# Performance work log

Measured on AMD Instinct MI355X. Metric: run time of the kernel, lower is better.

The kernel has to match this reference:

```python
import jax, jax.numpy as jnp
import numpy as np

B, T, E, H = 64, 577, 768, 64
GRID_H, GRID_W = 24, 24
NUM_PREFIX = 1
N = GRID_H * GRID_W  # 576 patches
EPS = 1e-5


def setup_inputs() -> dict:
    key = jax.random.key(0)
    ks = jax.random.split(key, 12)
    s = lambda k, shape, fan: jax.random.normal(k, shape, jnp.float32) / np.sqrt(fan)
    return {
        "x": jax.random.normal(ks[0], (B, T, E), jnp.float32),
        "w_q": s(ks[1], (E, H), E),
        "w_k": s(ks[2], (E, H), E),
        "w_v": s(ks[3], (E, H), E),
        "q_gamma": jnp.ones((H,), jnp.float32),
        "q_beta": jnp.zeros((H,), jnp.float32),
        "k_gamma": jnp.ones((H,), jnp.float32),
        "k_beta": jnp.zeros((H,), jnp.float32),
        "w_sigma": s(ks[4], (H, 2), H),
        "b_sigma": jnp.zeros((2,), jnp.float32),
        "w_alpha": s(ks[5], (H, 1), H),
        "b_alpha": jnp.zeros((1,), jnp.float32),
    }


def _layernorm(x, gamma, beta):
    mu = jnp.mean(x, axis=-1, keepdims=True)
    var = jnp.mean(jnp.square(x - mu), axis=-1, keepdims=True)
    return (x - mu) * jax.lax.rsqrt(var + EPS) * gamma + beta


def _grid_sq_dists():
    # coords[i] = (row, col) of patch i; squared coordinate differences [N, N]
    coords = jnp.stack(
        jnp.meshgrid(jnp.arange(GRID_H), jnp.arange(GRID_W), indexing="ij"), axis=-1
    ).reshape(N, 2).astype(jnp.float32)
    diff = coords[:, None, :] - coords[None, :, :]  # [N, N, 2]
    dy2 = jnp.square(diff[..., 0])  # row diff squared
    dx2 = jnp.square(diff[..., 1])  # col diff squared
    return dx2, dy2


def reference(x, w_q, w_k, w_v, q_gamma, q_beta, k_gamma, k_beta,
              w_sigma, b_sigma, w_alpha, b_alpha):
    q = _layernorm(x @ w_q, q_gamma, q_beta)  # [B, T, H]
    k = _layernorm(x @ w_k, k_gamma, k_beta)  # [B, T, H]
    v = x @ w_v                               # [B, T, H]

    sim = jnp.einsum("bqh,bkh->bqk", q, k)    # [B, T, T]

    q_nc = q[:, NUM_PREFIX:, :]               # [B, N, H]
    alpha = jax.nn.softplus(q_nc @ w_alpha + b_alpha)[..., 0]  # [B, N]
    sigma = jax.nn.sigmoid(q_nc @ w_sigma + b_sigma)           # [B, N, 2]
    sx = sigma[..., 0]  # [B, N]
    sy = sigma[..., 1]

    dx2, dy2 = _grid_sq_dists()  # [N, N] each
    # Gaussian decay bias: query-patch p controls sigma; [B, N, N]
    G = jnp.exp(
        -dx2[None] / (2.0 * jnp.square(sx)[:, :, None])
        - dy2[None] / (2.0 * jnp.square(sy)[:, :, None])
    )
    S = alpha[:, :, None] * G

    sim = sim.at[:, NUM_PREFIX:, NUM_PREFIX:].add(S)

    scale = jnp.sqrt(jnp.float32(H))
    attn = jax.nn.softmax(sim / scale, axis=-1)
    return attn @ v  # [B, T, H]
```

## Files before the change

kernel.cpp:

```cpp
#include <hip/hip_runtime.h>
#include <math.h>

#define B_ 64
#define T_ 577
#define E_ 768
#define H_ 64
#define N_ 576
#define GW_ 24

typedef float f32x4 __attribute__((ext_vector_type(4)));
typedef __bf16 bf16x8 __attribute__((ext_vector_type(8)));
typedef __bf16 bf16x4 __attribute__((ext_vector_type(4)));

__device__ inline void split_bf16(float f, __bf16& h, __bf16& l) {
  h = (__bf16)f;
  l = (__bf16)(f - (float)h);
}

__global__ __launch_bounds__(256) void prep_w_kernel(
    const float* __restrict__ wq, const float* __restrict__ wk, const float* __restrict__ wv,
    __bf16* __restrict__ wsw_hi, __bf16* __restrict__ wsw_lo)
{
  int t = blockIdx.x * 256 + threadIdx.x;
  if (t >= 24*192) return;
  int kc = t / 192, n = t - (t/192)*192;
  const float* src = (n < 64) ? wq : ((n < 128) ? wk : wv);
  int nn = n & 63;
  __bf16 hbuf[32], lbuf[32];
  #pragma unroll
  for (int kk = 0; kk < 32; ++kk) {
    float f = src[(size_t)(kc*32 + kk)*64 + nn];
    split_bf16(f, hbuf[kk], lbuf[kk]);
  }
  size_t base = (size_t)t * 32;
  #pragma unroll
  for (int i = 0; i < 4; ++i) {
    *(bf16x8*)(wsw_hi + base + i*8) = *(bf16x8*)&hbuf[i*8];
    *(bf16x8*)(wsw_lo + base + i*8) = *(bf16x8*)&lbuf[i*8];
  }
}

__global__ __launch_bounds__(256) void qkv_ln_kernel(
    const float* __restrict__ x,
    const __bf16* __restrict__ wsw_hi, const __bf16* __restrict__ wsw_lo,
    const float* __restrict__ qg, const float* __restrict__ qb,
    const float* __restrict__ kg, const float* __restrict__ kb,
    const float* __restrict__ wsig, const float* __restrict__ bsig,
    const float* __restrict__ walp, const float* __restrict__ balp,
    float* __restrict__ qo, float* __restrict__ ko, float* __restrict__ vo,
    float* __restrict__ alo, float* __restrict__ sxo, float* __restrict__ syo)
{
  __shared__ __align__(16) float smem[64*193 + 256];
  __bf16* A_hi = (__bf16*)smem;
  __bf16* A_lo = A_hi + 64*40;
  __bf16* B_hi = A_lo + 64*40;
  __bf16* B_lo = B_hi + 192*40;
  float (*Cs)[193] = (float (*)[193])smem;
  float* mu_q = smem + 64*193;
  float* rs_q = mu_q + 64;
  float* mu_k = rs_q + 64;
  float* rs_k = mu_k + 64;

  const int tid  = threadIdx.x;
  const int lane = tid & 63;
  const int w    = tid >> 6;
  const int rowbase = blockIdx.x << 6;

  f32x4 acc[4][3];
  #pragma unroll
  for (int mt = 0; mt < 4; ++mt)
    #pragma unroll
    for (int nt = 0; nt < 3; ++nt)
      acc[mt][nt] = (f32x4){0.f, 0.f, 0.f, 0.f};

  const int m     = lane & 15;
  const int kfrag = (lane >> 4) * 8;

  float4 xr0, xr1;
  bf16x8 whr[3], wlr[3];
  const int s0 = tid, s1 = tid + 256;
  const int arow0 = s0 >> 3, ak0 = (s0 & 7) * 4;
  const int arow1 = s1 >> 3, ak1 = (s1 & 7) * 4;

  auto load_chunk = [&](int kc) {
    xr0 = *(const float4*)(x + (size_t)(rowbase + arow0)*E_ + kc*32 + ak0);
    xr1 = *(const float4*)(x + (size_t)(rowbase + arow1)*E_ + kc*32 + ak1);
    #pragma unroll
    for (int i = 0; i < 3; ++i) {
      int e = tid + 256*i;
      whr[i] = *(const bf16x8*)(wsw_hi + (size_t)kc*6144 + e*8);
      wlr[i] = *(const bf16x8*)(wsw_lo + (size_t)kc*6144 + e*8);
    }
  };
  auto store_chunk = [&]() {
    __bf16 h0,l0,h1,l1,h2,l2,h3,l3;
    split_bf16(xr0.x,h0,l0); split_bf16(xr0.y,h1,l1);
    split_bf16(xr0.z,h2,l2); split_bf16(xr0.w,h3,l3);
    *(bf16x4*)&A_hi[arow0*40 + ak0] = (bf16x4){h0,h1,h2,h3};
    *(bf16x4*)&A_lo[arow0*40 + ak0] = (bf16x4){l0,l1,l2,l3};
    split_bf16(xr1.x,h0,l0); split_bf16(xr1.y,h1,l1);
    split_bf16(xr1.z,h2,l2); split_bf16(xr1.w,h3,l3);
    *(bf16x4*)&A_hi[arow1*40 + ak1] = (bf16x4){h0,h1,h2,h3};
    *(bf16x4*)&A_lo[arow1*40 + ak1] = (bf16x4){l0,l1,l2,l3};
    #pragma unroll
    for (int i = 0; i < 3; ++i) {
      int e = tid + 256*i;
      int n = e >> 2, g = e & 3;
      *(bf16x8*)&B_hi[n*40 + g*8] = whr[i];
      *(bf16x8*)&B_lo[n*40 + g*8] = wlr[i];
    }
  };

  load_chunk(0);
  #pragma unroll 1
  for (int kc = 0; kc < 24; ++kc) {
    __syncthreads();
    store_chunk();
    __syncthreads();
    if (kc < 23) load_chunk(kc + 1);

    bf16x8 bh[3], bl[3];
    #pragma unroll
    for (int nt = 0; nt < 3; ++nt) {
      int n = w*48 + nt*16 + m;
      bh[nt] = *(const bf16x8*)&B_hi[n*40 + kfrag];
      bl[nt] = *(const bf16x8*)&B_lo[n*40 + kfrag];
    }
    #pragma unroll
    for (int mt = 0; mt < 4; ++mt) {
      bf16x8 ah = *(const bf16x8*)&A_hi[(mt*16 + m)*40 + kfrag];
      bf16x8 al = *(const bf16x8*)&A_lo[(mt*16 + m)*40 + kfrag];
      #pragma unroll
      for (int nt = 0; nt < 3; ++nt) {
        acc[mt][nt] = __builtin_amdgcn_mfma_f32_16x16x32_bf16(ah, bh[nt], acc[mt][nt], 0, 0, 0);
        acc[mt][nt] = __builtin_amdgcn_mfma_f32_16x16x32_bf16(al, bh[nt], acc[mt][nt], 0, 0, 0);
        acc[mt][nt] = __builtin_amdgcn_mfma_f32_16x16x32_bf16(ah, bl[nt], acc[mt][nt], 0, 0, 0);
      }
    }
  }
  __syncthreads();

  #pragma unroll
  for (int mt = 0; mt < 4; ++mt)
    #pragma unroll
    for (int nt = 0; nt < 3; ++nt) {
      int row = mt*16 + (lane >> 4)*4;
      int col = w*48 + nt*16 + (lane & 15);
      Cs[row + 0][col] = acc[mt][nt].x;
      Cs[row + 1][col] = acc[mt][nt].y;
      Cs[row + 2][col] = acc[mt][nt].z;
      Cs[row + 3][col] = acc[mt][nt].w;
    }
  __syncthreads();

  if (tid < 64) {
    float s = 0.f;
    for (int h = 0; h < 64; ++h) s += Cs[tid][h];
    float mu = s * (1.f/64.f);
    float vs = 0.f;
    for (int h = 0; h < 64; ++h) { float d = Cs[tid][h] - mu; vs += d*d; }
    mu_q[tid] = mu;
    rs_q[tid] = rsqrtf(vs*(1.f/64.f) + 1e-5f);
  } else if (tid < 128) {
    int r = tid - 64;
    float s = 0.f;
    for (int h = 0; h < 64; ++h) s += Cs[r][64+h];
    float mu = s * (1.f/64.f);
    float vs = 0.f;
    for (int h = 0; h < 64; ++h) { float d = Cs[r][64+h] - mu; vs += d*d; }
    mu_k[r] = mu;
    rs_k[r] = rsqrtf(vs*(1.f/64.f) + 1e-5f);
  }
  __syncthreads();

  if (tid >= 192) {
    int r = tid - 192;
    int mrow = rowbase + r;
    int tindex = mrow % T_;
    if (tindex >= 1) {
      int bb = mrow / T_;
      int g = tindex - 1;
      float mu = mu_q[r], rs = rs_q[r];
      float za = 0.f, z0 = 0.f, z1 = 0.f;
      for (int h = 0; h < 64; ++h) {
        float qv = (Cs[r][h] - mu) * rs * qg[h] + qb[h];
        za += qv * walp[h];
        z0 += qv * wsig[2*h];
        z1 += qv * wsig[2*h+1];
      }
      za += balp[0]; z0 += bsig[0]; z1 += bsig[1];
      float al = fmaxf(za, 0.f) + log1pf(__expf(-fabsf(za)));
      float sx = 1.f/(1.f + __expf(-z0));
      float sy = 1.f/(1.f + __expf(-z1));
      alo[bb*N_ + g] = al;
      sxo[bb*N_ + g] = 0.5f/(sx*sx);
      syo[bb*N_ + g] = 0.5f/(sy*sy);
    }
  }
  for (int idx = tid; idx < 64*48; idx += 256) {
    int r = idx / 48, c4 = (idx - (idx/48)*48) * 4;
    size_t row = (size_t)rowbase + r;
    float4 val = make_float4(Cs[r][c4], Cs[r][c4+1], Cs[r][c4+2], Cs[r][c4+3]);
    if (c4 < 64) {
      float mu = mu_q[r], rs = rs_q[r];
      float4 o;
      o.x = (val.x - mu)*rs*qg[c4+0] + qb[c4+0];
      o.y = (val.y - mu)*rs*qg[c4+1] + qb[c4+1];
      o.z = (val.z - mu)*rs*qg[c4+2] + qb[c4+2];
      o.w = (val.w - mu)*rs*qg[c4+3] + qb[c4+3];
      *(float4*)(qo + row*64 + c4) = o;
    } else if (c4 < 128) {
      int h = c4 - 64;
      float mu = mu_k[r], rs = rs_k[r];
      float4 o;
      o.x = (val.x - mu)*rs*kg[h+0] + kb[h+0];
      o.y = (val.y - mu)*rs*kg[h+1] + kb[h+1];
      o.z = (val.z - mu)*rs*kg[h+2] + kb[h+2];
      o.w = (val.w - mu)*rs*kg[h+3] + kb[h+3];
      *(float4*)(ko + row*64 + h) = o;
    } else {
      *(float4*)(vo + row*64 + (c4-128)) = val;
    }
  }
}

__global__ __launch_bounds__(256) void attn_kernel(
    const float* __restrict__ q, const float* __restrict__ k, const float* __restrict__ v,
    const float* __restrict__ ala, const float* __restrict__ sxa, const float* __restrict__ sya,
    float* __restrict__ out)
{
  __shared__ __align__(16) __bf16 sm[8*4608];
  __shared__ float prm_al[64], prm_sx[64], prm_sy[64], prm_gr[64], prm_gc[64];
  __shared__ int   prm_has[64];

  __bf16* QH = sm;            __bf16* QL = sm + 4608;
  __bf16* KH = sm + 2*4608;   __bf16* KL = sm + 3*4608;
  __bf16* VH = sm + 4*4608;   __bf16* VL = sm + 5*4608;
  __bf16* PH = sm + 6*4608;   __bf16* PL = sm + 7*4608;

  const int tid  = threadIdx.x;
  const int lane = tid & 63;
  const int w    = tid >> 6;
  const int quad = lane >> 4;
  const int mrow = lane & 15;
  const int b    = blockIdx.y;
  const int qt   = blockIdx.x;

  const float* qbase = q + (size_t)b * T_ * H_;
  const float* kbase = k + (size_t)b * T_ * H_;
  const float* vbase = v + (size_t)b * T_ * H_;

  if (tid < 64) {
    int row = qt*64 + tid;
    float al=0.f, isx=0.f, isy=0.f, gr=0.f, gc=0.f; int has = 0;
    if (row >= 1 && row < T_) {
      int g = row - 1;
      al  = ala[b*N_ + g] * 0.125f;
      isx = sxa[b*N_ + g];
      isy = sya[b*N_ + g];
      gr  = (float)(g / GW_);
      gc  = (float)(g - (g/GW_)*GW_);
      has = 1;
    }
    prm_al[tid]=al; prm_sx[tid]=isx; prm_sy[tid]=isy;
    prm_gr[tid]=gr; prm_gc[tid]=gc; prm_has[tid]=has;
  }
  #pragma unroll
  for (int i = 0; i < 4; ++i) {
    int s = tid + 256*i;
    int r = s >> 4, c4 = (s & 15)*4;
    int row = qt*64 + r;
    int rowc = row < T_ ? row : T_ - 1;
    float4 v4 = *(const float4*)(qbase + (size_t)rowc*H_ + c4);
    v4.x *= 0.125f; v4.y *= 0.125f; v4.z *= 0.125f; v4.w *= 0.125f;
    __bf16 h0,l0,h1,l1,h2,l2,h3,l3;
    split_bf16(v4.x,h0,l0); split_bf16(v4.y,h1,l1);
    split_bf16(v4.z,h2,l2); split_bf16(v4.w,h3,l3);
    *(bf16x4*)&QH[r*72 + c4] = (bf16x4){h0,h1,h2,h3};
    *(bf16x4*)&QL[r*72 + c4] = (bf16x4){l0,l1,l2,l3};
  }
  __syncthreads();

  float p_al[4], p_sx[4], p_sy[4], p_gr[4], p_gc[4]; int p_has[4];
  #pragma unroll
  for (int reg = 0; reg < 4; ++reg) {
    int rr = w*16 + quad*4 + reg;
    p_al[reg]=prm_al[rr]; p_sx[reg]=prm_sx[rr]; p_sy[reg]=prm_sy[rr];
    p_gr[reg]=prm_gr[rr]; p_gc[reg]=prm_gc[rr]; p_has[reg]=prm_has[rr];
  }

  float mo[4], lsum[4], O_[4][4];
  #pragma unroll
  for (int reg = 0; reg < 4; ++reg) { mo[reg] = -INFINITY; lsum[reg] = 0.f; }
  #pragma unroll
  for (int nt = 0; nt < 4; ++nt)
    #pragma unroll
    for (int reg = 0; reg < 4; ++reg) O_[nt][reg] = 0.f;

  float4 kreg[4];
  float  vreg[16];
  const int d0 = tid & 15, k0 = (tid >> 4) * 4;

  auto load_kv = [&](int kt) {
    #pragma unroll
    for (int i = 0; i < 4; ++i) {
      int s = tid + 256*i;
      int key = s >> 4, c4 = (s & 15)*4;
      int kgl = kt*64 + key;
      int kcl = kgl < T_ ? kgl : T_ - 1;
      kreg[i] = *(const float4*)(kbase + (size_t)kcl*H_ + c4);
    }
    #pragma unroll
    for (int di = 0; di < 4; ++di)
      #pragma unroll
      for (int ki = 0; ki < 4; ++ki) {
        int kgl = kt*64 + k0 + ki;
        int kcl = kgl < T_ ? kgl : T_ - 1;
        vreg[di*4+ki] = vbase[(size_t)kcl*H_ + d0 + 16*di];
      }
  };
  auto store_kv = [&]() {
    #pragma unroll
    for (int i = 0; i < 4; ++i) {
      int s = tid + 256*i;
      int key = s >> 4, c4 = (s & 15)*4;
      __bf16 h0,l0,h1,l1,h2,l2,h3,l3;
      split_bf16(kreg[i].x,h0,l0); split_bf16(kreg[i].y,h1,l1);
      split_bf16(kreg[i].z,h2,l2); split_bf16(kreg[i].w,h3,l3);
      *(bf16x4*)&KH[key*72 + c4] = (bf16x4){h0,h1,h2,h3};
      *(bf16x4*)&KL[key*72 + c4] = (bf16x4){l0,l1,l2,l3};
    }
    #pragma unroll
    for (int di = 0; di < 4; ++di) {
      int dim = d0 + 16*di;
      __bf16 h0,l0,h1,l1,h2,l2,h3,l3;
      split_bf16(vreg[di*4+0],h0,l0); split_bf16(vreg[di*4+1],h1,l1);
      split_bf16(vreg[di*4+2],h2,l2); split_bf16(vreg[di*4+3],h3,l3);
      *(bf16x4*)&VH[dim*72 + k0] = (bf16x4){h0,h1,h2,h3};
      *(bf16x4*)&VL[dim*72 + k0] = (bf16x4){l0,l1,l2,l3};
    }
  };

  load_kv(0);
  #pragma unroll 1
  for (int kt = 0; kt < 10; ++kt) {
    __syncthreads();
    store_kv();
    __syncthreads();
    if (kt < 9) load_kv(kt + 1);

    float S_[4][4];
    {
      f32x4 sac[4];
      #pragma unroll
      for (int nt = 0; nt < 4; ++nt) sac[nt] = (f32x4){0.f,0.f,0.f,0.f};
      #pragma unroll
      for (int ks = 0; ks < 2; ++ks) {
        int ko_ = ks*32 + quad*8;
        bf16x8 qh = *(const bf16x8*)&QH[(w*16 + mrow)*72 + ko_];
        bf16x8 ql = *(const bf16x8*)&QL[(w*16 + mrow)*72 + ko_];
        #pragma unroll
        for (int nt = 0; nt < 4; ++nt) {
          bf16x8 kh = *(const bf16x8*)&KH[(nt*16 + mrow)*72 + ko_];
          bf16x8 kl = *(const bf16x8*)&KL[(nt*16 + mrow)*72 + ko_];
          sac[nt] = __builtin_amdgcn_mfma_f32_16x16x32_bf16(qh, kh, sac[nt], 0, 0, 0);
          sac[nt] = __builtin_amdgcn_mfma_f32_16x16x32_bf16(ql, kh, sac[nt], 0, 0, 0);
          sac[nt] = __builtin_amdgcn_mfma_f32_16x16x32_bf16(qh, kl, sac[nt], 0, 0, 0);
        }
      }
      #pragma unroll
      for (int nt = 0; nt < 4; ++nt) {
        S_[nt][0] = sac[nt].x; S_[nt][1] = sac[nt].y;
        S_[nt][2] = sac[nt].z; S_[nt][3] = sac[nt].w;
      }
    }

    #pragma unroll
    for (int nt = 0; nt < 4; ++nt) {
      int keyg = kt*64 + nt*16 + mrow;
      bool kval = keyg < T_;
      bool khas = (keyg >= 1) && kval;
      float kgf = (float)(keyg - 1);
      float krf = floorf(kgf * (1.0f/24.0f));
      float kcf = kgf - 24.f*krf;
      #pragma unroll
      for (int reg = 0; reg < 4; ++reg) {
        float sval = S_[nt][reg];
        float dx = p_gc[reg] - kcf, dy = p_gr[reg] - krf;
        float bias = p_al[reg] * __expf(-(dx*dx*p_sx[reg] + dy*dy*p_sy[reg]));
        sval += (khas && p_has[reg]) ? bias : 0.f;
        S_[nt][reg] = kval ? sval : -1e30f;
      }
    }

    float lt_[4], sc_[4], mn_[4];
    #pragma unroll
    for (int reg = 0; reg < 4; ++reg) {
      float mx = fmaxf(fmaxf(S_[0][reg], S_[1][reg]), fmaxf(S_[2][reg], S_[3][reg]));
      mx = fmaxf(mx, __shfl_xor(mx, 1, 64));
      mx = fmaxf(mx, __shfl_xor(mx, 2, 64));
      mx = fmaxf(mx, __shfl_xor(mx, 4, 64));
      mx = fmaxf(mx, __shfl_xor(mx, 8, 64));
      mn_[reg] = fmaxf(mo[reg], mx);
      lt_[reg] = 0.f;
    }
    #pragma unroll
    for (int nt = 0; nt < 4; ++nt)
      #pragma unroll
      for (int reg = 0; reg < 4; ++reg) {
        float p = __expf(S_[nt][reg] - mn_[reg]);
        S_[nt][reg] = p;
        lt_[reg] += p;
      }
    #pragma unroll
    for (int reg = 0; reg < 4; ++reg) {
      float ls = lt_[reg];
      ls += __shfl_xor(ls, 1, 64);
      ls += __shfl_xor(ls, 2, 64);
      ls += __shfl_xor(ls, 4, 64);
      ls += __shfl_xor(ls, 8, 64);
      sc_[reg] = __expf(mo[reg] - mn_[reg]);
      lsum[reg] = lsum[reg]*sc_[reg] + ls;
      mo[reg] = mn_[reg];
    }
    #pragma unroll
    for (int nt = 0; nt < 4; ++nt)
      #pragma unroll
      for (int reg = 0; reg < 4; ++reg) O_[nt][reg] *= sc_[reg];

    #pragma unroll
    for (int nt = 0; nt < 4; ++nt)
      #pragma unroll
      for (int reg = 0; reg < 4; ++reg) {
        float p = S_[nt][reg];
        __bf16 ph, pl;
        split_bf16(p, ph, pl);
        int addr = (w*16 + quad*4 + reg)*72 + nt*16 + mrow;
        PH[addr] = ph;
        PL[addr] = pl;
      }

    #pragma unroll
    for (int nt = 0; nt < 4; ++nt) {
      f32x4 c = (f32x4){O_[nt][0], O_[nt][1], O_[nt][2], O_[nt][3]};
      #pragma unroll
      for (int ks = 0; ks < 2; ++ks) {
        int ko_ = ks*32 + quad*8;
        bf16x8 pah  = *(const bf16x8*)&PH[(w*16 + mrow)*72 + ko_];
        bf16x8 pall = *(const bf16x8*)&PL[(w*16 + mrow)*72 + ko_];
        bf16x8 vh   = *(const bf16x8*)&VH[(nt*16 + mrow)*72 + ko_];
        bf16x8 vl   = *(const bf16x8*)&VL[(nt*16 + mrow)*72 + ko_];
        c = __builtin_amdgcn_mfma_f32_16x16x32_bf16(pah, vh, c, 0, 0, 0);
        c = __builtin_amdgcn_mfma_f32_16x16x32_bf16(pall, vh, c, 0, 0, 0);
        c = __builtin_amdgcn_mfma_f32_16x16x32_bf16(pah, vl, c, 0, 0, 0);
      }
      O_[nt][0] = c.x; O_[nt][1] = c.y; O_[nt][2] = c.z; O_[nt][3] = c.w;
    }
  }

  #pragma unroll
  for (int reg = 0; reg < 4; ++reg) {
    int rowg = qt*64 + w*16 + quad*4 + reg;
    if (rowg < T_) {
      float inv = 1.f / lsum[reg];
      #pragma unroll
      for (int nt = 0; nt < 4; ++nt) {
        out[((size_t)b*T_ + rowg)*H_ + nt*16 + mrow] = O_[nt][reg] * inv;
      }
    }
  }
}

extern "C" void kernel_launch(void* const* d_in, const int* in_sizes, int n_in,
                              void* d_out, int out_size, void* d_ws, size_t ws_size,
                              hipStream_t stream) {
  const float* x      = (const float*)d_in[0];
  const float* wq     = (const float*)d_in[1];
  const float* wk     = (const float*)d_in[2];
  const float* wv     = (const float*)d_in[3];
  const float* qg     = (const float*)d_in[4];
  const float* qb     = (const float*)d_in[5];
  const float* kg     = (const float*)d_in[6];
  const float* kb     = (const float*)d_in[7];
  const float* wsig   = (const float*)d_in[8];
  const float* bsig   = (const float*)d_in[9];
  const float* walp   = (const float*)d_in[10];
  const float* balp   = (const float*)d_in[11];
  float* out = (float*)d_out;

  float* ws  = (float*)d_ws;
  const size_t nrow = (size_t)B_ * T_;
  float* qo  = ws;
  float* ko  = qo + nrow*H_;
  float* vo  = ko + nrow*H_;
  float* alo = vo + nrow*H_;
  float* sxo = alo + (size_t)B_*N_;
  float* syo = sxo + (size_t)B_*N_;
  __bf16* wsw_hi = (__bf16*)(syo + (size_t)B_*N_);
  __bf16* wsw_lo = wsw_hi + 24*192*32;

  hipLaunchKernelGGL(prep_w_kernel, dim3(18), dim3(256), 0, stream,
                     wq, wk, wv, wsw_hi, wsw_lo);
  hipLaunchKernelGGL(qkv_ln_kernel, dim3(577), dim3(256), 0, stream,
                     x, wsw_hi, wsw_lo, qg, qb, kg, kb, wsig, bsig, walp, balp,
                     qo, ko, vo, alo, sxo, syo);
  hipLaunchKernelGGL(attn_kernel, dim3(10, B_), dim3(256), 0, stream,
                     qo, ko, vo, alo, sxo, syo, out);
}
```

Measured before the change: 290.1 us.

## Keep Q and P in registers via transposed MFMA and bpermute

The attention kernel now computes S transposed (K as the A operand, Q as the B operand), so each lane owns a single query row. Q fragments stay in registers and the P tile is rebuilt for the PV MFMA with ds_bpermute instead of going through shared memory. This removes the Q/P shared buffers, halves LDS use, simplifies the row reductions to two cross-quad shuffles, and sets launch bounds to 4 blocks per CU. The trade-off is more VGPRs per thread and extra bpermute and select instructions per tile.

```diff
diff --git a/kernel.cpp b/kernel.cpp
--- a/kernel.cpp
+++ b/kernel.cpp
@@ -15,6 +15,10 @@
 __device__ inline void split_bf16(float f, __bf16& h, __bf16& l) {
   h = (__bf16)f;
   l = (__bf16)(f - (float)h);
+}
+
+__device__ inline float bperm_f(int byte_addr, float x) {
+  return __int_as_float(__builtin_amdgcn_ds_bpermute(byte_addr, __float_as_int(x)));
 }
 
 __global__ __launch_bounds__(256) void prep_w_kernel(
@@ -224,25 +228,20 @@
   }
 }
 
-__global__ __launch_bounds__(256) void attn_kernel(
+__global__ __launch_bounds__(256, 4) void attn_kernel(
     const float* __restrict__ q, const float* __restrict__ k, const float* __restrict__ v,
     const float* __restrict__ ala, const float* __restrict__ sxa, const float* __restrict__ sya,
     float* __restrict__ out)
 {
-  __shared__ __align__(16) __bf16 sm[8*4608];
-  __shared__ float prm_al[64], prm_sx[64], prm_sy[64], prm_gr[64], prm_gc[64];
-  __shared__ int   prm_has[64];
-
-  __bf16* QH = sm;            __bf16* QL = sm + 4608;
-  __bf16* KH = sm + 2*4608;   __bf16* KL = sm + 3*4608;
-  __bf16* VH = sm + 4*4608;   __bf16* VL = sm + 5*4608;
-  __bf16* PH = sm + 6*4608;   __bf16* PL = sm + 7*4608;
+  __shared__ __align__(16) __bf16 sm[4*4608];
+  __bf16* KH = sm;            __bf16* KL = sm + 4608;
+  __bf16* VH = sm + 2*4608;   __bf16* VL = sm + 3*4608;
 
   const int tid  = threadIdx.x;
   const int lane = tid & 63;
   const int w    = tid >> 6;
   const int quad = lane >> 4;
-  const int mrow = lane & 15;
+  const int m    = lane & 15;
   const int b    = blockIdx.y;
   const int qt   = blockIdx.x;
 
@@ -250,52 +249,47 @@
   const float* kbase = k + (size_t)b * T_ * H_;
   const float* vbase = v + (size_t)b * T_ * H_;
 
-  if (tid < 64) {
-    int row = qt*64 + tid;
-    float al=0.f, isx=0.f, isy=0.f, gr=0.f, gc=0.f; int has = 0;
-    if (row >= 1 && row < T_) {
-      int g = row - 1;
+  const int  row    = qt*64 + w*16 + m;
+  const int  rowc   = row < T_ ? row : T_ - 1;
+  const bool qvalid = row < T_;
+  const bool qhas   = (row >= 1) && qvalid;
+  float al = 0.f, isx = 0.f, isy = 0.f, qr = 0.f, qc = 0.f;
+  {
+    int g = qhas ? row - 1 : 0;
+    if (qhas) {
       al  = ala[b*N_ + g] * 0.125f;
       isx = sxa[b*N_ + g];
       isy = sya[b*N_ + g];
-      gr  = (float)(g / GW_);
-      gc  = (float)(g - (g/GW_)*GW_);
-      has = 1;
-    }
-    prm_al[tid]=al; prm_sx[tid]=isx; prm_sy[tid]=isy;
-    prm_gr[tid]=gr; prm_gc[tid]=gc; prm_has[tid]=has;
-  }
-  #pragma unroll
-  for (int i = 0; i < 4; ++i) {
-    int s = tid + 256*i;
-    int r = s >> 4, c4 = (s & 15)*4;
-    int row = qt*64 + r;
-    int rowc = row < T_ ? row : T_ - 1;
-    float4 v4 = *(const float4*)(qbase + (size_t)rowc*H_ + c4);
-    v4.x *= 0.125f; v4.y *= 0.125f; v4.z *= 0.125f; v4.w *= 0.125f;
-    __bf16 h0,l0,h1,l1,h2,l2,h3,l3;
-    split_bf16(v4.x,h0,l0); split_bf16(v4.y,h1,l1);
-    split_bf16(v4.z,h2,l2); split_bf16(v4.w,h3,l3);
-    *(bf16x4*)&QH[r*72 + c4] = (bf16x4){h0,h1,h2,h3};
-    *(bf16x4*)&QL[r*72 + c4] = (bf16x4){l0,l1,l2,l3};
-  }
-  __syncthreads();
-
-  float p_al[4], p_sx[4], p_sy[4], p_gr[4], p_gc[4]; int p_has[4];
-  #pragma unroll
-  for (int reg = 0; reg < 4; ++reg) {
-    int rr = w*16 + quad*4 + reg;
-    p_al[reg]=prm_al[rr]; p_sx[reg]=prm_sx[rr]; p_sy[reg]=prm_sy[rr];
-    p_gr[reg]=prm_gr[rr]; p_gc[reg]=prm_gc[rr]; p_has[reg]=prm_has[rr];
-  }
-
-  float mo[4], lsum[4], O_[4][4];
-  #pragma unroll
-  for (int reg = 0; reg < 4; ++reg) { mo[reg] = -INFINITY; lsum[reg] = 0.f; }
-  #pragma unroll
-  for (int nt = 0; nt < 4; ++nt)
-    #pragma unroll
-    for (int reg = 0; reg < 4; ++reg) O_[nt][reg] = 0.f;
+      int gr = g / GW_;
+      qr = (float)gr;
+      qc = (float)(g - gr*GW_);
+    }
+  }
+
+  bf16x8 qh[2], ql[2];
+  #pragma unroll
+  for (int ks = 0; ks < 2; ++ks) {
+    float4 f0 = *(const float4*)(qbase + (size_t)rowc*H_ + ks*32 + quad*8);
+    float4 f1 = *(const float4*)(qbase + (size_t)rowc*H_ + ks*32 + quad*8 + 4);
+    float fv[8] = {f0.x, f0.y, f0.z, f0.w, f1.x, f1.y, f1.z, f1.w};
+    #pragma unroll
+    for (int j = 0; j < 8; ++j) {
+      float s = fv[j] * 0.125f;
+      __bf16 h, l;
+      split_bf16(s, h, l);
+      qh[ks][j] = h;
+      ql[ks][j] = l;
+    }
+  }
+
+  float mo = -INFINITY, lsum = 0.f;
+  f32x4 acc[4];
+  #pragma unroll
+  for (int nt = 0; nt < 4; ++nt) acc[nt] = (f32x4){0.f, 0.f, 0.f, 0.f};
+
+  const int  addrA = ((2*(quad & 1))*16 + m) * 4;
+  const int  addrB = addrA + 64;
+  const bool hiNT  = quad >= 2;
 
   float4 kreg[4];
   float  vreg[16];
@@ -349,124 +343,110 @@
     __syncthreads();
     if (kt < 9) load_kv(kt + 1);
 
-    float S_[4][4];
-    {
-      f32x4 sac[4];
-      #pragma unroll
-      for (int nt = 0; nt < 4; ++nt) sac[nt] = (f32x4){0.f,0.f,0.f,0.f};
+    float s_[4][4];
+    #pragma unroll
+    for (int nt = 0; nt < 4; ++nt) {
+      f32x4 sac = (f32x4){0.f, 0.f, 0.f, 0.f};
       #pragma unroll
       for (int ks = 0; ks < 2; ++ks) {
-        int ko_ = ks*32 + quad*8;
-        bf16x8 qh = *(const bf16x8*)&QH[(w*16 + mrow)*72 + ko_];
-        bf16x8 ql = *(const bf16x8*)&QL[(w*16 + mrow)*72 + ko_];
-        #pragma unroll
-        for (int nt = 0; nt < 4; ++nt) {
-          bf16x8 kh = *(const bf16x8*)&KH[(nt*16 + mrow)*72 + ko_];
-          bf16x8 kl = *(const bf16x8*)&KL[(nt*16 + mrow)*72 + ko_];
-          sac[nt] = __builtin_amdgcn_mfma_f32_16x16x32_bf16(qh, kh, sac[nt], 0, 0, 0);
-          sac[nt] = __builtin_amdgcn_mfma_f32_16x16x32_bf16(ql, kh, sac[nt], 0, 0, 0);
-          sac[nt] = __builtin_amdgcn_mfma_f32_16x16x32_bf16(qh, kl, sac[nt], 0, 0, 0);
-        }
-      }
-      #pragma unroll
-      for (int nt = 0; nt < 4; ++nt) {
-        S_[nt][0] = sac[nt].x; S_[nt][1] = sac[nt].y;
-        S_[nt][2] = sac[nt].z; S_[nt][3] = sac[nt].w;
-      }
+        const int ko_ = ks*32 + quad*8;
+        bf16x8 kh = *(const bf16x8*)&KH[(nt*16 + m)*72 + ko_];
+        bf16x8 kl = *(const bf16x8*)&KL[(nt*16 + m)*72 + ko_];
+        sac = __builtin_amdgcn_mfma_f32_16x16x32_bf16(kh, qh[ks], sac, 0, 0, 0);
+        sac = __builtin_amdgcn_mfma_f32_16x16x32_bf16(kl, qh[ks], sac, 0, 0, 0);
+        sac = __builtin_amdgcn_mfma_f32_16x16x32_bf16(kh, ql[ks], sac, 0, 0, 0);
+      }
+      s_[nt][0] = sac.x; s_[nt][1] = sac.y; s_[nt][2] = sac.z; s_[nt][3] = sac.w;
     }
 
     #pragma unroll
     for (int nt = 0; nt < 4; ++nt) {
-      int keyg = kt*64 + nt*16 + mrow;
-      bool kval = keyg < T_;
-      bool khas = (keyg >= 1) && kval;
-      float kgf = (float)(keyg - 1);
-      float krf = floorf(kgf * (1.0f/24.0f));
-      float kcf = kgf - 24.f*krf;
       #pragma unroll
       for (int reg = 0; reg < 4; ++reg) {
-        float sval = S_[nt][reg];
-        float dx = p_gc[reg] - kcf, dy = p_gr[reg] - krf;
-        float bias = p_al[reg] * __expf(-(dx*dx*p_sx[reg] + dy*dy*p_sy[reg]));
-        sval += (khas && p_has[reg]) ? bias : 0.f;
-        S_[nt][reg] = kval ? sval : -1e30f;
-      }
-    }
-
-    float lt_[4], sc_[4], mn_[4];
-    #pragma unroll
-    for (int reg = 0; reg < 4; ++reg) {
-      float mx = fmaxf(fmaxf(S_[0][reg], S_[1][reg]), fmaxf(S_[2][reg], S_[3][reg]));
-      mx = fmaxf(mx, __shfl_xor(mx, 1, 64));
-      mx = fmaxf(mx, __shfl_xor(mx, 2, 64));
-      mx = fmaxf(mx, __shfl_xor(mx, 4, 64));
-      mx = fmaxf(mx, __shfl_xor(mx, 8, 64));
-      mn_[reg] = fmaxf(mo[reg], mx);
-      lt_[reg] = 0.f;
-    }
+        int key = kt*64 + nt*16 + quad*4 + reg;
+        float sval = s_[nt][reg];
+        float kgf = (float)(key - 1);
+        float krf = floorf(kgf * (1.0f/24.0f));
+        float kcf = kgf - 24.f*krf;
+        float dx = qc - kcf, dy = qr - krf;
+        float bias = al * __expf(-(dx*dx*isx + dy*dy*isy));
+        bool khas = (key >= 1) && (key < T_);
+        sval += (khas && qhas) ? bias : 0.f;
+        s_[nt][reg] = (key < T_) ? sval : -1e30f;
+      }
+    }
+
+    float mx = s_[0][0];
     #pragma unroll
     for (int nt = 0; nt < 4; ++nt)
       #pragma unroll
+      for (int reg = 0; reg < 4; ++reg)
+        mx = fmaxf(mx, s_[nt][reg]);
+    mx = fmaxf(mx, __shfl_xor(mx, 16, 64));
+    mx = fmaxf(mx, __shfl_xor(mx, 32, 64));
+    float mn = fmaxf(mo, mx);
+    float sc = __expf(mo - mn);
+    float lt = 0.f;
+    #pragma unroll
+    for (int nt = 0; nt < 4; ++nt)
+      #pragma unroll
       for (int reg = 0; reg < 4; ++reg) {
-        float p = __expf(S_[nt][reg] - mn_[reg]);
-        S_[nt][reg] = p;
-        lt_[reg] += p;
-      }
-    #pragma unroll
-    for (int reg = 0; reg < 4; ++reg) {
-      float ls = lt_[reg];
-      ls += __shfl_xor(ls, 1, 64);
-      ls += __shfl_xor(ls, 2, 64);
-      ls += __shfl_xor(ls, 4, 64);
-      ls += __shfl_xor(ls, 8, 64);
-      sc_[reg] = __expf(mo[reg] - mn_[reg]);
-      lsum[reg] = lsum[reg]*sc_[reg] + ls;
-      mo[reg] = mn_[reg];
-    }
-    #pragma unroll
-    for (int nt = 0; nt < 4; ++nt)
-      #pragma unroll
-      for (int reg = 0; reg < 4; ++reg) O_[nt][reg] *= sc_[reg];
-
-    #pragma unroll
-    for (int nt = 0; nt < 4; ++nt)
+        float p = __expf(s_[nt][reg] - mn);
+        s_[nt][reg] = p;
+        lt += p;
+      }
+    lt += __shfl_xor(lt, 16, 64);
+    lt += __shfl_xor(lt, 32, 64);
+    lsum = lsum*sc + lt;
+    mo = mn;
+    #pragma unroll
+    for (int nt = 0; nt < 4; ++nt) {
+      acc[nt].x *= sc; acc[nt].y *= sc; acc[nt].z *= sc; acc[nt].w *= sc;
+    }
+
+    bf16x8 fh[2], fl[2];
+    #pragma unroll
+    for (int ks = 0; ks < 2; ++ks) {
       #pragma unroll
       for (int reg = 0; reg < 4; ++reg) {
-        float p = S_[nt][reg];
-        __bf16 ph, pl;
-        split_bf16(p, ph, pl);
-        int addr = (w*16 + quad*4 + reg)*72 + nt*16 + mrow;
-        PH[addr] = ph;
-        PL[addr] = pl;
-      }
+        float xa0 = bperm_f(addrA, s_[2*ks+0][reg]);
+        float xa1 = bperm_f(addrA, s_[2*ks+1][reg]);
+        float xb0 = bperm_f(addrB, s_[2*ks+0][reg]);
+        float xb1 = bperm_f(addrB, s_[2*ks+1][reg]);
+        float va = hiNT ? xa1 : xa0;
+        float vb = hiNT ? xb1 : xb0;
+        __bf16 h, l;
+        split_bf16(va, h, l); fh[ks][reg]   = h; fl[ks][reg]   = l;
+        split_bf16(vb, h, l); fh[ks][4+reg] = h; fl[ks][4+reg] = l;
+      }
+    }
 
     #pragma unroll
     for (int nt = 0; nt < 4; ++nt) {
-      f32x4 c = (f32x4){O_[nt][0], O_[nt][1], O_[nt][2], O_[nt][3]};
+      f32x4 c = acc[nt];
       #pragma unroll
       for (int ks = 0; ks < 2; ++ks) {
-        int ko_ = ks*32 + quad*8;
-        bf16x8 pah  = *(const bf16x8*)&PH[(w*16 + mrow)*72 + ko_];
-        bf16x8 pall = *(const bf16x8*)&PL[(w*16 + mrow)*72 + ko_];
-        bf16x8 vh   = *(const bf16x8*)&VH[(nt*16 + mrow)*72 + ko_];
-        bf16x8 vl   = *(const bf16x8*)&VL[(nt*16 + mrow)*72 + ko_];
-        c = __builtin_amdgcn_mfma_f32_16x16x32_bf16(pah, vh, c, 0, 0, 0);
-        c = __builtin_amdgcn_mfma_f32_16x16x32_bf16(pall, vh, c, 0, 0, 0);
-        c = __builtin_amdgcn_mfma_f32_16x16x32_bf16(pah, vl, c, 0, 0, 0);
-      }
-      O_[nt][0] = c.x; O_[nt][1] = c.y; O_[nt][2] = c.z; O_[nt][3] = c.w;
-    }
-  }
-
-  #pragma unroll
-  for (int reg = 0; reg < 4; ++reg) {
-    int rowg = qt*64 + w*16 + quad*4 + reg;
-    if (rowg < T_) {
-      float inv = 1.f / lsum[reg];
-      #pragma unroll
-      for (int nt = 0; nt < 4; ++nt) {
-        out[((size_t)b*T_ + rowg)*H_ + nt*16 + mrow] = O_[nt][reg] * inv;
-      }
+        const int ko_ = ks*32 + quad*8;
+        bf16x8 vh = *(const bf16x8*)&VH[(nt*16 + m)*72 + ko_];
+        bf16x8 vl = *(const bf16x8*)&VL[(nt*16 + m)*72 + ko_];
+        c = __builtin_amdgcn_mfma_f32_16x16x32_bf16(vh, fh[ks], c, 0, 0, 0);
+        c = __builtin_amdgcn_mfma_f32_16x16x32_bf16(vl, fh[ks], c, 0, 0, 0);
+        c = __builtin_amdgcn_mfma_f32_16x16x32_bf16(vh, fl[ks], c, 0, 0, 0);
+      }
+      acc[nt] = c;
+    }
+  }
+
+  if (qvalid) {
+    float inv = 1.f / lsum;
+    #pragma unroll
+    for (int nt = 0; nt < 4; ++nt) {
+      float4 o;
+      o.x = acc[nt].x * inv;
+      o.y = acc[nt].y * inv;
+      o.z = acc[nt].z * inv;
+      o.w = acc[nt].w * inv;
+      *(float4*)(out + ((size_t)b*T_ + row)*H_ + nt*16 + quad*4) = o;
     }
   }
 }
```

Measured after the change: 292.5 us. About the same (+0.8%).
